# Performance work log

Hardware: AMD Instinct MI355X
Metric: run time of the kernel (lower is better)

Reference implementation:

```python
import jax, jax.numpy as jnp
import numpy as np

N_JETS = 1024
DEPTH = 10
FEATURES = 8
HIDDEN = 128


def setup_inputs() -> dict:
    key = jax.random.key(0)
    keys = jax.random.split(key, DEPTH + 4)
    inp = {}
    for j in range(DEPTH):
        n = N_JETS * (2 ** j)
        inp["contents_%d" % j] = jax.random.normal(keys[j], (n, FEATURES), dtype=jnp.float32)
    for j in range(DEPTH - 1):
        n = N_JETS * (2 ** j)
        # complete binary tree: children of node i at level j are nodes 2i, 2i+1 at level j+1
        inp["children_%d" % j] = jnp.arange(2 * n, dtype=jnp.int32).reshape(n, 2)
    inp["W_u"] = jax.random.normal(keys[DEPTH], (HIDDEN, FEATURES), dtype=jnp.float32) * (1.0 / np.sqrt(FEATURES))
    inp["b_u"] = jnp.zeros((HIDDEN,), dtype=jnp.float32)
    inp["W_h"] = jax.random.normal(keys[DEPTH + 1], (HIDDEN, 3 * HIDDEN), dtype=jnp.float32) * (1.0 / np.sqrt(3 * HIDDEN))
    inp["b_h"] = jnp.zeros((HIDDEN,), dtype=jnp.float32)
    return inp


def _forward(contents, children, W_u, b_u, W_h, b_h):
    # Bottom-up pass: deepest level (leaves) first, exactly as the torch loop
    # over levels[::-1]. All non-leaf nodes are inner (n_inners[j] == n_j).
    emb = None
    L = len(contents)
    for j in reversed(range(L)):
        u = jax.nn.relu(contents[j] @ W_u.T + b_u)  # [n_j, H], fc_u + relu
        if j == L - 1:
            emb = u  # leaf level: no children, embedding is just u_k
        else:
            h_L = emb[children[j][:, 0]]  # gather left child embeddings  [n_j, H]
            h_R = emb[children[j][:, 1]]  # gather right child embeddings [n_j, H]
            h = jnp.concatenate([h_L, h_R, u], axis=1)  # [n_j, 3H]
            emb = jax.nn.relu(h @ W_h.T + b_h)  # fc_h + relu -> [n_j, H]
    return emb.reshape(N_JETS, -1)  # roots, one embedding per jet


def reference(contents_0, contents_1, contents_2, contents_3, contents_4,
              contents_5, contents_6, contents_7, contents_8, contents_9,
              children_0, children_1, children_2, children_3, children_4,
              children_5, children_6, children_7, children_8,
              W_u, b_u, W_h, b_h):
    contents = [contents_0, contents_1, contents_2, contents_3, contents_4,
                contents_5, contents_6, contents_7, contents_8, contents_9]
    children = [children_0, children_1, children_2, children_3, children_4,
                children_5, children_6, children_7, children_8]
    return _forward(contents, children, W_u, b_u, W_h, b_h)
```

## Files before the change

### kernel.cpp

```cpp
#include <hip/hip_runtime.h>
#include <hip/hip_bf16.h>

typedef __attribute__((ext_vector_type(8))) short bf16x8;
typedef __attribute__((ext_vector_type(4))) float f32x4;
typedef __attribute__((ext_vector_type(4))) unsigned short u16x4;

__device__ __forceinline__ unsigned short f2bf(float f) {
    __hip_bfloat16 h = __float2bfloat16(f);
    union { __hip_bfloat16 h; unsigned short u; } v; v.h = h;
    return v.u;
}

__device__ __forceinline__ void cp16_g2l(const void* g, void* l) {
    __builtin_amdgcn_global_load_lds(
        (const __attribute__((address_space(1))) unsigned int*)g,
        (__attribute__((address_space(3))) unsigned int*)l, 16, 0, 0);
}

__global__ __launch_bounds__(384) void k_cvtW(const float* __restrict__ Wh,
                                              unsigned short* __restrict__ Wbf) {
    int n = blockIdx.x, k = threadIdx.x;
    Wbf[n * 384 + k] = f2bf(Wh[n * 384 + k]);
}

__global__ __launch_bounds__(512, 4) void k_main(
    const float* __restrict__ c0, const float* __restrict__ c1,
    const float* __restrict__ c2, const float* __restrict__ c3,
    const float* __restrict__ c4, const float* __restrict__ c5,
    const float* __restrict__ c6, const float* __restrict__ c7,
    const float* __restrict__ c8, const float* __restrict__ c9,
    const unsigned short* __restrict__ Wbf,
    const float* __restrict__ Wu, const float* __restrict__ bu,
    const float* __restrict__ bh,
    unsigned short* __restrict__ tbase,
    float* __restrict__ outF)
{
    __shared__ __align__(16) unsigned short A_lds[2][64][128];
    __shared__ __align__(16) unsigned short u_lds[64][128];
    __shared__ __align__(16) unsigned short wu_lds[8][32][8];

    const int t = threadIdx.x, lane = t & 63, wid = t >> 6;
    const int l15 = lane & 15, l4 = lane >> 4;
    const int wrow = wid & 3;
    const int wcolh = wid >> 2;
    const int b = blockIdx.x;

    bf16x8 wreg[12];
    {
        int n = wid * 16 + l15;
        #pragma unroll
        for (int kb = 0; kb < 12; ++kb)
            wreg[kb] = *reinterpret_cast<const bf16x8*>(Wbf + n * 384 + kb * 32 + l4 * 8);
    }
    #pragma unroll
    for (int kb = 0; kb < 12; ++kb)
        asm volatile("" : "+v"(wreg[kb]));

    if (wid == 0 && l4 < 2) {
        #pragma unroll
        for (int nf = 0; nf < 8; ++nf) {
            int n = nf * 16 + l15;
            bf16x8 v = {0, 0, 0, 0, 0, 0, 0, 0};
            if (l4 == 0) {
                #pragma unroll
                for (int k = 0; k < 8; ++k) ((unsigned short*)&v)[k] = f2bf(Wu[n * 8 + k]);
            } else {
                ((unsigned short*)&v)[0] = f2bf(bu[n]);
            }
            *(bf16x8*)&wu_lds[nf][l4 * 16 + l15][0] = v;
        }
    }
    const f32x4 bh4 = *(const f32x4*)&bh[wid * 16 + l4 * 4];

    bf16x8 zeroA = {0, 0, 0, 0, 0, 0, 0, 0};
    bf16x8 onesA = zeroA; ((unsigned short*)&onesA)[0] = 0x3F80;

    __syncthreads();

    #define RG(j) (tbase + (size_t)131072 * (512 - (2 << (j))))

    f32x4 cO0 = {0,0,0,0}, cO1 = {0,0,0,0};

    {
        const int T = 8;
        const int tb = b * T;
        unsigned short* eOut = RG(8);
        if (l4 == 0) {
            const float* p = c8 + ((size_t)tb * 64 + wrow * 16 + l15) * 8;
            cO0 = *(const f32x4*)p; cO1 = *(const f32x4*)(p + 4);
        }
        for (int tt = 0; tt < T; ++tt) {
            const int tile = tb + tt;
            {
                bf16x8 cb = zeroA;
                if (l4 == 0) {
                    #pragma unroll
                    for (int e = 0; e < 4; ++e) {
                        ((unsigned short*)&cb)[e]     = f2bf(cO0[e]);
                        ((unsigned short*)&cb)[e + 4] = f2bf(cO1[e]);
                    }
                } else if (l4 == 1) cb = onesA;
                const int i = wrow * 16 + l15;
                #pragma unroll
                for (int nfi = 0; nfi < 4; ++nfi) {
                    int nf = wcolh * 4 + nfi;
                    bf16x8 wv = zeroA;
                    if (l4 < 2) wv = *(const bf16x8*)&wu_lds[nf][l4 * 16 + l15][0];
                    f32x4 z = {0.f, 0.f, 0.f, 0.f};
                    z = __builtin_amdgcn_mfma_f32_16x16x32_bf16(wv, cb, z, 0, 0, 0);
                    u16x4 pk;
                    #pragma unroll
                    for (int r = 0; r < 4; ++r) pk[r] = f2bf(fmaxf(z[r], 0.f));
                    int n4 = nf * 16 + l4 * 4;
                    *(u16x4*)&u_lds[i][n4 ^ ((i & 15) << 3)] = pk;
                }
            }
            {
                const float* pcBase = c9 + ((size_t)tile * 128 + wrow * 32 + l15) * 8;
                #pragma unroll
                for (int rb = 0; rb < 2; ++rb) {
                    bf16x8 cb = zeroA;
                    if (l4 == 0) {
                        f32x4 a  = *(const f32x4*)(pcBase + rb * 128);
                        f32x4 b2 = *(const f32x4*)(pcBase + rb * 128 + 4);
                        #pragma unroll
                        for (int e = 0; e < 4; ++e) {
                            ((unsigned short*)&cb)[e]     = f2bf(a[e]);
                            ((unsigned short*)&cb)[e + 4] = f2bf(b2[e]);
                        }
                    } else if (l4 == 1) cb = onesA;
                    const int rr = wrow * 32 + rb * 16 + l15;
                    const int cc = rr & 1, il = rr >> 1;
                    #pragma unroll
                    for (int nfi = 0; nfi < 4; ++nfi) {
                        int nf = wcolh * 4 + nfi;
                        bf16x8 wv = zeroA;
                        if (l4 < 2) wv = *(const bf16x8*)&wu_lds[nf][l4 * 16 + l15][0];
                        f32x4 z = {0.f, 0.f, 0.f, 0.f};
                        z = __builtin_amdgcn_mfma_f32_16x16x32_bf16(wv, cb, z, 0, 0, 0);
                        u16x4 pk;
                        #pragma unroll
                        for (int r = 0; r < 4; ++r) pk[r] = f2bf(fmaxf(z[r], 0.f));
                        int n4 = nf * 16 + l4 * 4;
                        *(u16x4*)&A_lds[cc][il][n4 ^ ((il & 15) << 3)] = pk;
                    }
                }
            }
            {
                int tn = (tt + 1 < T) ? tile + 1 : tile;
                if (l4 == 0) {
                    const float* p = c8 + ((size_t)tn * 64 + wrow * 16 + l15) * 8;
                    cO0 = *(const f32x4*)p; cO1 = *(const f32x4*)(p + 4);
                }
            }
            asm volatile("s_waitcnt lgkmcnt(0)" ::: "memory");
            __builtin_amdgcn_sched_barrier(0);
            __builtin_amdgcn_s_barrier();
            __builtin_amdgcn_sched_barrier(0);

            f32x4 acc[4];
            #pragma unroll
            for (int mf = 0; mf < 4; ++mf) acc[mf] = bh4;
            #pragma unroll
            for (int kb = 0; kb < 8; ++kb) {
                bf16x8 af[4];
                #pragma unroll
                for (int mf = 0; mf < 4; ++mf) {
                    int i = mf * 16 + l15;
                    af[mf] = *(const bf16x8*)&A_lds[kb >> 2][i][((((kb & 3) * 4) + l4) ^ (i & 15)) * 8];
                }
                #pragma unroll
                for (int mf = 0; mf < 4; ++mf)
                    acc[mf] = __builtin_amdgcn_mfma_f32_16x16x32_bf16(wreg[kb], af[mf], acc[mf], 0, 0, 0);
            }
            #pragma unroll
            for (int kb = 8; kb < 12; ++kb) {
                bf16x8 af[4];
                #pragma unroll
                for (int mf = 0; mf < 4; ++mf) {
                    int i = mf * 16 + l15;
                    af[mf] = *(const bf16x8*)&u_lds[i][((((kb - 8) * 4) + l4) ^ (i & 15)) * 8];
                }
                #pragma unroll
                for (int mf = 0; mf < 4; ++mf)
                    acc[mf] = __builtin_amdgcn_mfma_f32_16x16x32_bf16(wreg[kb], af[mf], acc[mf], 0, 0, 0);
            }
            #pragma unroll
            for (int mf = 0; mf < 4; ++mf) {
                int i = mf * 16 + l15;
                int Rg = tile * 64 + i;
                int rr = Rg & 127, cc = rr & 1, il = rr >> 1;
                u16x4 pk;
                #pragma unroll
                for (int r = 0; r < 4; ++r) pk[r] = f2bf(fmaxf(acc[mf][r], 0.f));
                int n4 = wid * 16 + l4 * 4;
                *(u16x4*)&eOut[(size_t)(Rg >> 7) * 16384 + cc * 8192 + il * 128
                               + (n4 ^ ((il & 15) << 3))] = pk;
            }
            asm volatile("s_waitcnt lgkmcnt(0)" ::: "memory");
            __builtin_amdgcn_sched_barrier(0);
            __builtin_amdgcn_s_barrier();
        }
        asm volatile("s_waitcnt vmcnt(0) lgkmcnt(0)" ::: "memory");
        __builtin_amdgcn_sched_barrier(0);
        __builtin_amdgcn_s_barrier();
    }

    for (int j = 7; j >= 5; --j) {
        const int T = 1 << (j - 5);
        const int tb = b * T;
        const float* contO = (j == 7) ? c7 : (j == 6) ? c6 : c5;
        const unsigned short* eIn = RG(j + 1);
        unsigned short* eOut = RG(j);

        {
            const unsigned short* src = eIn + (size_t)tb * 16384;
            #pragma unroll
            for (int it = 0; it < 4; ++it) {
                int q = t + it * 512;
                cp16_g2l(src + q * 8, &A_lds[0][0][0] + q * 8);
            }
            if (l4 == 0) {
                const float* p = contO + ((size_t)tb * 64 + wrow * 16 + l15) * 8;
                cO0 = *(const f32x4*)p; cO1 = *(const f32x4*)(p + 4);
            }
        }
        __syncthreads();

        for (int tt = 0; tt < T; ++tt) {
            const int tile = tb + tt;
            {
                bf16x8 cb = zeroA;
                if (l4 == 0) {
                    #pragma unroll
                    for (int e = 0; e < 4; ++e) {
                        ((unsigned short*)&cb)[e]     = f2bf(cO0[e]);
                        ((unsigned short*)&cb)[e + 4] = f2bf(cO1[e]);
                    }
                } else if (l4 == 1) cb = onesA;
                const int i = wrow * 16 + l15;
                #pragma unroll
                for (int nfi = 0; nfi < 4; ++nfi) {
                    int nf = wcolh * 4 + nfi;
                    bf16x8 wv = zeroA;
                    if (l4 < 2) wv = *(const bf16x8*)&wu_lds[nf][l4 * 16 + l15][0];
                    f32x4 z = {0.f, 0.f, 0.f, 0.f};
                    z = __builtin_amdgcn_mfma_f32_16x16x32_bf16(wv, cb, z, 0, 0, 0);
                    u16x4 pk;
                    #pragma unroll
                    for (int r = 0; r < 4; ++r) pk[r] = f2bf(fmaxf(z[r], 0.f));
                    int n4 = nf * 16 + l4 * 4;
                    *(u16x4*)&u_lds[i][n4 ^ ((i & 15) << 3)] = pk;
                }
            }
            {
                int tn = (tt + 1 < T) ? tile + 1 : tile;
                if (l4 == 0) {
                    const float* p = contO + ((size_t)tn * 64 + wrow * 16 + l15) * 8;
                    cO0 = *(const f32x4*)p; cO1 = *(const f32x4*)(p + 4);
                }
            }
            asm volatile("s_waitcnt vmcnt(6)" ::: "memory");
            asm volatile("s_waitcnt lgkmcnt(0)" ::: "memory");
            __builtin_amdgcn_sched_barrier(0);
            __builtin_amdgcn_s_barrier();
            __builtin_amdgcn_sched_barrier(0);

            f32x4 acc[4];
            #pragma unroll
            for (int mf = 0; mf < 4; ++mf) acc[mf] = bh4;
            #pragma unroll
            for (int kb = 0; kb < 8; ++kb) {
                bf16x8 af[4];
                #pragma unroll
                for (int mf = 0; mf < 4; ++mf) {
                    int i = mf * 16 + l15;
                    af[mf] = *(const bf16x8*)&A_lds[kb >> 2][i][((((kb & 3) * 4) + l4) ^ (i & 15)) * 8];
                }
                #pragma unroll
                for (int mf = 0; mf < 4; ++mf)
                    acc[mf] = __builtin_amdgcn_mfma_f32_16x16x32_bf16(wreg[kb], af[mf], acc[mf], 0, 0, 0);
            }
            asm volatile("s_waitcnt lgkmcnt(0)" ::: "memory");
            __builtin_amdgcn_sched_barrier(0);
            __builtin_amdgcn_s_barrier();
            __builtin_amdgcn_sched_barrier(0);
            if (tt + 1 < T) {
                const unsigned short* src = eIn + (size_t)(tile + 1) * 16384;
                #pragma unroll
                for (int it = 0; it < 4; ++it) {
                    int q = t + it * 512;
                    cp16_g2l(src + q * 8, &A_lds[0][0][0] + q * 8);
                }
            }
            #pragma unroll
            for (int kb = 8; kb < 12; ++kb) {
                bf16x8 af[4];
                #pragma unroll
                for (int mf = 0; mf < 4; ++mf) {
                    int i = mf * 16 + l15;
                    af[mf] = *(const bf16x8*)&u_lds[i][((((kb - 8) * 4) + l4) ^ (i & 15)) * 8];
                }
                #pragma unroll
                for (int mf = 0; mf < 4; ++mf)
                    acc[mf] = __builtin_amdgcn_mfma_f32_16x16x32_bf16(wreg[kb], af[mf], acc[mf], 0, 0, 0);
            }
            #pragma unroll
            for (int mf = 0; mf < 4; ++mf) {
                int i = mf * 16 + l15;
                int Rg = tile * 64 + i;
                int rr = Rg & 127, cc = rr & 1, il = rr >> 1;
                u16x4 pk;
                #pragma unroll
                for (int r = 0; r < 4; ++r) pk[r] = f2bf(fmaxf(acc[mf][r], 0.f));
                int n4 = wid * 16 + l4 * 4;
                *(u16x4*)&eOut[(size_t)(Rg >> 7) * 16384 + cc * 8192 + il * 128
                               + (n4 ^ ((il & 15) << 3))] = pk;
            }
            asm volatile("s_waitcnt lgkmcnt(0)" ::: "memory");
            __builtin_amdgcn_sched_barrier(0);
            __builtin_amdgcn_s_barrier();
        }
        asm volatile("s_waitcnt vmcnt(0) lgkmcnt(0)" ::: "memory");
        __builtin_amdgcn_sched_barrier(0);
        __builtin_amdgcn_s_barrier();
    }

    for (int j = 4; j >= 0; --j) {
        const int R = 2 << j;
        const float* contO = (j == 4) ? c4 : (j == 3) ? c3 : (j == 2) ? c2
                           : (j == 1) ? c1 : c0;
        const unsigned short* eIn = RG(j + 1);
        unsigned short* eOut = (j > 0) ? RG(j) : nullptr;

        const size_t rowBase  = (size_t)b * (size_t)R;
        const size_t crowBase = rowBase * 2;

        {
            const int ilBase = ((int)(crowBase & 127)) >> 1;
            const unsigned short* gb = eIn + (crowBase >> 7) * (size_t)16384
                                     + (size_t)ilBase * 128;
            const int per = R * 16;
            for (int q = t; q < 2 * per; q += 512) {
                int cc = (q >= per) ? 1 : 0;
                int qq = q - cc * per;
                int il = qq >> 4, slot = qq & 15;
                int kc  = slot ^ (il & 15);
                int src = kc ^ ((ilBase + il) & 15);
                bf16x8 v = *(const bf16x8*)(gb + (size_t)cc * 8192 + il * 128 + src * 8);
                *(bf16x8*)&A_lds[cc][il][slot * 8] = v;
            }
        }
        {
            f32x4 a0 = {0,0,0,0}, a1 = {0,0,0,0};
            if (l4 == 0) {
                size_t row = rowBase + (size_t)(wrow * 16 + l15);
                size_t mx = rowBase + R - 1; if (row > mx) row = mx;
                const float* p = contO + row * 8;
                a0 = *(const f32x4*)p; a1 = *(const f32x4*)(p + 4);
            }
            bf16x8 cb = zeroA;
            if (l4 == 0) {
                #pragma unroll
                for (int e = 0; e < 4; ++e) {
                    ((unsigned short*)&cb)[e]     = f2bf(a0[e]);
                    ((unsigned short*)&cb)[e + 4] = f2bf(a1[e]);
                }
            } else if (l4 == 1) cb = onesA;
            const int i = wrow * 16 + l15;
            #pragma unroll
            for (int nfi = 0; nfi < 4; ++nfi) {
                int nf = wcolh * 4 + nfi;
                bf16x8 wv = zeroA;
                if (l4 < 2) wv = *(const bf16x8*)&wu_lds[nf][l4 * 16 + l15][0];
                f32x4 z = {0.f, 0.f, 0.f, 0.f};
                z = __builtin_amdgcn_mfma_f32_16x16x32_bf16(wv, cb, z, 0, 0, 0);
                u16x4 pk;
                #pragma unroll
                for (int r = 0; r < 4; ++r) pk[r] = f2bf(fmaxf(z[r], 0.f));
                int n4 = nf * 16 + l4 * 4;
                *(u16x4*)&u_lds[i][n4 ^ ((i & 15) << 3)] = pk;
            }
        }
        asm volatile("s_waitcnt lgkmcnt(0)" ::: "memory");
        __builtin_amdgcn_sched_barrier(0);
        __builtin_amdgcn_s_barrier();
        __builtin_amdgcn_sched_barrier(0);

        f32x4 acc[4];
        #pragma unroll
        for (int mf = 0; mf < 4; ++mf) acc[mf] = bh4;
        #pragma unroll
        for (int kb = 0; kb < 8; ++kb) {
            bf16x8 af[4];
            #pragma unroll
            for (int mf = 0; mf < 4; ++mf) {
                int i = mf * 16 + l15;
                af[mf] = *(const bf16x8*)&A_lds[kb >> 2][i][((((kb & 3) * 4) + l4) ^ (i & 15)) * 8];
            }
            #pragma unroll
            for (int mf = 0; mf < 4; ++mf)
                acc[mf] = __builtin_amdgcn_mfma_f32_16x16x32_bf16(wreg[kb], af[mf], acc[mf], 0, 0, 0);
        }
        #pragma unroll
        for (int kb = 8; kb < 12; ++kb) {
            bf16x8 af[4];
            #pragma unroll
            for (int mf = 0; mf < 4; ++mf) {
                int i = mf * 16 + l15;
                af[mf] = *(const bf16x8*)&u_lds[i][((((kb - 8) * 4) + l4) ^ (i & 15)) * 8];
            }
            #pragma unroll
            for (int mf = 0; mf < 4; ++mf)
                acc[mf] = __builtin_amdgcn_mfma_f32_16x16x32_bf16(wreg[kb], af[mf], acc[mf], 0, 0, 0);
        }
        if (j == 0) {
            #pragma unroll
            for (int mf = 0; mf < 4; ++mf) {
                int i = mf * 16 + l15;
                if (i < R) {
                    f32x4 o;
                    #pragma unroll
                    for (int r = 0; r < 4; ++r) o[r] = fmaxf(acc[mf][r], 0.f);
                    *(f32x4*)&outF[(rowBase + i) * 128 + wid * 16 + l4 * 4] = o;
                }
            }
        } else {
            #pragma unroll
            for (int mf = 0; mf < 4; ++mf) {
                int i = mf * 16 + l15;
                if (i < R) {
                    size_t Rg = rowBase + i;
                    int rr = (int)(Rg & 127), cc = rr & 1, il = rr >> 1;
                    u16x4 pk;
                    #pragma unroll
                    for (int r = 0; r < 4; ++r) pk[r] = f2bf(fmaxf(acc[mf][r], 0.f));
                    int n4 = wid * 16 + l4 * 4;
                    *(u16x4*)&eOut[(Rg >> 7) * 16384 + cc * 8192 + il * 128
                                   + (n4 ^ ((il & 15) << 3))] = pk;
                }
            }
        }
        asm volatile("s_waitcnt vmcnt(0) lgkmcnt(0)" ::: "memory");
        __builtin_amdgcn_sched_barrier(0);
        __builtin_amdgcn_s_barrier();
    }
    #undef RG
}

extern "C" void kernel_launch(void* const* d_in, const int* in_sizes, int n_in,
                              void* d_out, int out_size, void* d_ws, size_t ws_size,
                              hipStream_t stream) {
    const float* c[10];
    for (int j = 0; j < 10; ++j) c[j] = (const float*)d_in[j];
    const float* Wu = (const float*)d_in[19];
    const float* bu = (const float*)d_in[20];
    const float* Wh = (const float*)d_in[21];
    const float* bh = (const float*)d_in[22];

    unsigned short* Wbf   = (unsigned short*)d_ws;
    unsigned short* tbase = (unsigned short*)((char*)d_ws + (1u << 20));

    k_cvtW<<<128, 384, 0, stream>>>(Wh, Wbf);
    k_main<<<512, 512, 0, stream>>>(c[0], c[1], c[2], c[3], c[4], c[5], c[6], c[7],
                                    c[8], c[9], Wbf, Wu, bu, bh, tbase, (float*)d_out);
}
```

Measured before the change: 125.2 us.

## Fuse level 8 into level 7 via LDS, keep W_u in registers

Level-8 embeddings are now computed into a second LDS buffer and consumed directly by the level-7 GEMM in the same block, so the level-8 global round trip and its phase disappear. W_u and bias fragments are held in registers instead of being read from LDS on every small MFMA, and repeated code is factored into lambdas. The cost is a larger LDS footprint, which may lower occupancy, plus extra barriers per sub-tile.

```diff
diff --git a/kernel.cpp b/kernel.cpp
--- a/kernel.cpp
+++ b/kernel.cpp
@@ -35,14 +35,13 @@
     unsigned short* __restrict__ tbase,
     float* __restrict__ outF)
 {
-    __shared__ __align__(16) unsigned short A_lds[2][64][128];
+    __shared__ __align__(16) unsigned short A_c9[2][64][128];
+    __shared__ __align__(16) unsigned short A8[2][64][128];
     __shared__ __align__(16) unsigned short u_lds[64][128];
-    __shared__ __align__(16) unsigned short wu_lds[8][32][8];
 
     const int t = threadIdx.x, lane = t & 63, wid = t >> 6;
     const int l15 = lane & 15, l4 = lane >> 4;
-    const int wrow = wid & 3;
-    const int wcolh = wid >> 2;
+    const int wrow = wid & 3, wcolh = wid >> 2;
     const int b = blockIdx.x;
 
     bf16x8 wreg[12];
@@ -56,39 +55,189 @@
     for (int kb = 0; kb < 12; ++kb)
         asm volatile("" : "+v"(wreg[kb]));
 
-    if (wid == 0 && l4 < 2) {
-        #pragma unroll
-        for (int nf = 0; nf < 8; ++nf) {
-            int n = nf * 16 + l15;
-            bf16x8 v = {0, 0, 0, 0, 0, 0, 0, 0};
-            if (l4 == 0) {
-                #pragma unroll
-                for (int k = 0; k < 8; ++k) ((unsigned short*)&v)[k] = f2bf(Wu[n * 8 + k]);
-            } else {
-                ((unsigned short*)&v)[0] = f2bf(bu[n]);
-            }
-            *(bf16x8*)&wu_lds[nf][l4 * 16 + l15][0] = v;
-        }
-    }
+    bf16x8 wureg[4];
+    #pragma unroll
+    for (int nfi = 0; nfi < 4; ++nfi) {
+        int n = (wcolh * 4 + nfi) * 16 + l15;
+        bf16x8 v = {0, 0, 0, 0, 0, 0, 0, 0};
+        if (l4 == 0) {
+            #pragma unroll
+            for (int k = 0; k < 8; ++k) ((unsigned short*)&v)[k] = f2bf(Wu[n * 8 + k]);
+        } else if (l4 == 1) {
+            ((unsigned short*)&v)[0] = f2bf(bu[n]);
+        }
+        wureg[nfi] = v;
+    }
+    #pragma unroll
+    for (int nfi = 0; nfi < 4; ++nfi)
+        asm volatile("" : "+v"(wureg[nfi]));
+
     const f32x4 bh4 = *(const f32x4*)&bh[wid * 16 + l4 * 4];
-
     bf16x8 zeroA = {0, 0, 0, 0, 0, 0, 0, 0};
     bf16x8 onesA = zeroA; ((unsigned short*)&onesA)[0] = 0x3F80;
 
-    __syncthreads();
-
     #define RG(j) (tbase + (size_t)131072 * (512 - (2 << (j))))
-
-    f32x4 cO0 = {0,0,0,0}, cO1 = {0,0,0,0};
+    #define BAR_LGKM() do { asm volatile("s_waitcnt lgkmcnt(0)" ::: "memory"); \
+        __builtin_amdgcn_sched_barrier(0); __builtin_amdgcn_s_barrier(); \
+        __builtin_amdgcn_sched_barrier(0); } while (0)
+
+    auto UPH = [&](const float* contO, size_t row0, size_t rowMax) {
+        bf16x8 cb = zeroA;
+        if (l4 == 0) {
+            size_t row = row0 + (size_t)(wrow * 16 + l15);
+            if (row > rowMax) row = rowMax;
+            const float* p = contO + row * 8;
+            f32x4 a0 = *(const f32x4*)p, a1 = *(const f32x4*)(p + 4);
+            #pragma unroll
+            for (int e = 0; e < 4; ++e) {
+                ((unsigned short*)&cb)[e]     = f2bf(a0[e]);
+                ((unsigned short*)&cb)[e + 4] = f2bf(a1[e]);
+            }
+        } else if (l4 == 1) cb = onesA;
+        const int i = wrow * 16 + l15;
+        #pragma unroll
+        for (int nfi = 0; nfi < 4; ++nfi) {
+            f32x4 z = {0.f, 0.f, 0.f, 0.f};
+            z = __builtin_amdgcn_mfma_f32_16x16x32_bf16(wureg[nfi], cb, z, 0, 0, 0);
+            u16x4 pk;
+            #pragma unroll
+            for (int r = 0; r < 4; ++r) pk[r] = f2bf(fmaxf(z[r], 0.f));
+            int n4 = (wcolh * 4 + nfi) * 16 + l4 * 4;
+            *(u16x4*)&u_lds[i][n4 ^ ((i & 15) << 3)] = pk;
+        }
+    };
+    auto GEMM_A = [&](const unsigned short (*A)[64][128], f32x4* acc) {
+        #pragma unroll
+        for (int mf = 0; mf < 4; ++mf) acc[mf] = bh4;
+        #pragma unroll
+        for (int kb = 0; kb < 8; ++kb) {
+            bf16x8 af[4];
+            #pragma unroll
+            for (int mf = 0; mf < 4; ++mf) {
+                int i = mf * 16 + l15;
+                af[mf] = *(const bf16x8*)&A[kb >> 2][i][((((kb & 3) * 4) + l4) ^ (i & 15)) * 8];
+            }
+            #pragma unroll
+            for (int mf = 0; mf < 4; ++mf)
+                acc[mf] = __builtin_amdgcn_mfma_f32_16x16x32_bf16(wreg[kb], af[mf], acc[mf], 0, 0, 0);
+        }
+    };
+    auto GEMM_U = [&](f32x4* acc) {
+        #pragma unroll
+        for (int kb = 8; kb < 12; ++kb) {
+            bf16x8 af[4];
+            #pragma unroll
+            for (int mf = 0; mf < 4; ++mf) {
+                int i = mf * 16 + l15;
+                af[mf] = *(const bf16x8*)&u_lds[i][((((kb - 8) * 4) + l4) ^ (i & 15)) * 8];
+            }
+            #pragma unroll
+            for (int mf = 0; mf < 4; ++mf)
+                acc[mf] = __builtin_amdgcn_mfma_f32_16x16x32_bf16(wreg[kb], af[mf], acc[mf], 0, 0, 0);
+        }
+    };
 
     {
-        const int T = 8;
+        unsigned short* e7 = RG(7);
+        for (int q = 0; q < 4; ++q) {
+            const int tile7 = b * 4 + q;
+            for (int s = 0; s < 2; ++s) {
+                const size_t tile8 = (size_t)tile7 * 2 + s;
+                UPH(c8, tile8 * 64, tile8 * 64 + 63);
+                {
+                    const float* pcBase = c9 + (tile8 * 128 + (size_t)(wrow * 32 + l15)) * 8;
+                    #pragma unroll
+                    for (int rb = 0; rb < 2; ++rb) {
+                        bf16x8 cb = zeroA;
+                        if (l4 == 0) {
+                            f32x4 a  = *(const f32x4*)(pcBase + rb * 128);
+                            f32x4 b2 = *(const f32x4*)(pcBase + rb * 128 + 4);
+                            #pragma unroll
+                            for (int e = 0; e < 4; ++e) {
+                                ((unsigned short*)&cb)[e]     = f2bf(a[e]);
+                                ((unsigned short*)&cb)[e + 4] = f2bf(b2[e]);
+                            }
+                        } else if (l4 == 1) cb = onesA;
+                        const int rr = wrow * 32 + rb * 16 + l15;
+                        const int cc = rr & 1, il = rr >> 1;
+                        #pragma unroll
+                        for (int nfi = 0; nfi < 4; ++nfi) {
+                            f32x4 z = {0.f, 0.f, 0.f, 0.f};
+                            z = __builtin_amdgcn_mfma_f32_16x16x32_bf16(wureg[nfi], cb, z, 0, 0, 0);
+                            u16x4 pk;
+                            #pragma unroll
+                            for (int r = 0; r < 4; ++r) pk[r] = f2bf(fmaxf(z[r], 0.f));
+                            int n4 = (wcolh * 4 + nfi) * 16 + l4 * 4;
+                            *(u16x4*)&A_c9[cc][il][n4 ^ ((il & 15) << 3)] = pk;
+                        }
+                    }
+                }
+                BAR_LGKM();
+                {
+                    f32x4 acc[4];
+                    GEMM_A(A_c9, acc);
+                    GEMM_U(acc);
+                    #pragma unroll
+                    for (int mf = 0; mf < 4; ++mf) {
+                        int i = mf * 16 + l15;
+                        int cc = i & 1, il = s * 32 + (i >> 1);
+                        u16x4 pk;
+                        #pragma unroll
+                        for (int r = 0; r < 4; ++r) pk[r] = f2bf(fmaxf(acc[mf][r], 0.f));
+                        int n4 = wid * 16 + l4 * 4;
+                        *(u16x4*)&A8[cc][il][n4 ^ ((il & 15) << 3)] = pk;
+                    }
+                }
+                BAR_LGKM();
+            }
+            UPH(c7, (size_t)tile7 * 64, (size_t)tile7 * 64 + 63);
+            BAR_LGKM();
+            {
+                f32x4 acc[4];
+                GEMM_A(A8, acc);
+                GEMM_U(acc);
+                #pragma unroll
+                for (int mf = 0; mf < 4; ++mf) {
+                    int i = mf * 16 + l15;
+                    int Rg = tile7 * 64 + i;
+                    int rr = Rg & 127, cc = rr & 1, il = rr >> 1;
+                    u16x4 pk;
+                    #pragma unroll
+                    for (int r = 0; r < 4; ++r) pk[r] = f2bf(fmaxf(acc[mf][r], 0.f));
+                    int n4 = wid * 16 + l4 * 4;
+                    *(u16x4*)&e7[(size_t)(Rg >> 7) * 16384 + cc * 8192 + il * 128
+                                 + (n4 ^ ((il & 15) << 3))] = pk;
+                }
+            }
+            BAR_LGKM();
+        }
+        asm volatile("s_waitcnt vmcnt(0) lgkmcnt(0)" ::: "memory");
+        __builtin_amdgcn_sched_barrier(0);
+        __builtin_amdgcn_s_barrier();
+    }
+
+    for (int j = 6; j >= 5; --j) {
+        const int T = 1 << (j - 5);
         const int tb = b * T;
-        unsigned short* eOut = RG(8);
-        if (l4 == 0) {
-            const float* p = c8 + ((size_t)tb * 64 + wrow * 16 + l15) * 8;
-            cO0 = *(const f32x4*)p; cO1 = *(const f32x4*)(p + 4);
-        }
+        const float* contO = (j == 6) ? c6 : c5;
+        const unsigned short* eIn = RG(j + 1);
+        unsigned short* eOut = RG(j);
+
+        f32x4 cO0 = {0,0,0,0}, cO1 = {0,0,0,0};
+        {
+            const unsigned short* src = eIn + (size_t)tb * 16384;
+            #pragma unroll
+            for (int it = 0; it < 4; ++it) {
+                int q = t + it * 512;
+                cp16_g2l(src + q * 8, &A_c9[0][0][0] + q * 8);
+            }
+            if (l4 == 0) {
+                const float* p = contO + ((size_t)tb * 64 + wrow * 16 + l15) * 8;
+                cO0 = *(const f32x4*)p; cO1 = *(const f32x4*)(p + 4);
+            }
+        }
+        __syncthreads();
+
         for (int tt = 0; tt < T; ++tt) {
             const int tile = tb + tt;
             {
@@ -103,153 +252,12 @@
                 const int i = wrow * 16 + l15;
                 #pragma unroll
                 for (int nfi = 0; nfi < 4; ++nfi) {
-                    int nf = wcolh * 4 + nfi;
-                    bf16x8 wv = zeroA;
-                    if (l4 < 2) wv = *(const bf16x8*)&wu_lds[nf][l4 * 16 + l15][0];
                     f32x4 z = {0.f, 0.f, 0.f, 0.f};
-                    z = __builtin_amdgcn_mfma_f32_16x16x32_bf16(wv, cb, z, 0, 0, 0);
+                    z = __builtin_amdgcn_mfma_f32_16x16x32_bf16(wureg[nfi], cb, z, 0, 0, 0);
                     u16x4 pk;
                     #pragma unroll
                     for (int r = 0; r < 4; ++r) pk[r] = f2bf(fmaxf(z[r], 0.f));
-                    int n4 = nf * 16 + l4 * 4;
-                    *(u16x4*)&u_lds[i][n4 ^ ((i & 15) << 3)] = pk;
-                }
-            }
-            {
-                const float* pcBase = c9 + ((size_t)tile * 128 + wrow * 32 + l15) * 8;
-                #pragma unroll
-                for (int rb = 0; rb < 2; ++rb) {
-                    bf16x8 cb = zeroA;
-                    if (l4 == 0) {
-                        f32x4 a  = *(const f32x4*)(pcBase + rb * 128);
-                        f32x4 b2 = *(const f32x4*)(pcBase + rb * 128 + 4);
-                        #pragma unroll
-                        for (int e = 0; e < 4; ++e) {
-                            ((unsigned short*)&cb)[e]     = f2bf(a[e]);
-                            ((unsigned short*)&cb)[e + 4] = f2bf(b2[e]);
-                        }
-                    } else if (l4 == 1) cb = onesA;
-                    const int rr = wrow * 32 + rb * 16 + l15;
-                    const int cc = rr & 1, il = rr >> 1;
-                    #pragma unroll
-                    for (int nfi = 0; nfi < 4; ++nfi) {
-                        int nf = wcolh * 4 + nfi;
-                        bf16x8 wv = zeroA;
-                        if (l4 < 2) wv = *(const bf16x8*)&wu_lds[nf][l4 * 16 + l15][0];
-                        f32x4 z = {0.f, 0.f, 0.f, 0.f};
-                        z = __builtin_amdgcn_mfma_f32_16x16x32_bf16(wv, cb, z, 0, 0, 0);
-                        u16x4 pk;
-                        #pragma unroll
-                        for (int r = 0; r < 4; ++r) pk[r] = f2bf(fmaxf(z[r], 0.f));
-                        int n4 = nf * 16 + l4 * 4;
-                        *(u16x4*)&A_lds[cc][il][n4 ^ ((il & 15) << 3)] = pk;
-                    }
-                }
-            }
-            {
-                int tn = (tt + 1 < T) ? tile + 1 : tile;
-                if (l4 == 0) {
-                    const float* p = c8 + ((size_t)tn * 64 + wrow * 16 + l15) * 8;
-                    cO0 = *(const f32x4*)p; cO1 = *(const f32x4*)(p + 4);
-                }
-            }
-            asm volatile("s_waitcnt lgkmcnt(0)" ::: "memory");
-            __builtin_amdgcn_sched_barrier(0);
-            __builtin_amdgcn_s_barrier();
-            __builtin_amdgcn_sched_barrier(0);
-
-            f32x4 acc[4];
-            #pragma unroll
-            for (int mf = 0; mf < 4; ++mf) acc[mf] = bh4;
-            #pragma unroll
-            for (int kb = 0; kb < 8; ++kb) {
-                bf16x8 af[4];
-                #pragma unroll
-                for (int mf = 0; mf < 4; ++mf) {
-                    int i = mf * 16 + l15;
-                    af[mf] = *(const bf16x8*)&A_lds[kb >> 2][i][((((kb & 3) * 4) + l4) ^ (i & 15)) * 8];
-                }
-                #pragma unroll
-                for (int mf = 0; mf < 4; ++mf)
-                    acc[mf] = __builtin_amdgcn_mfma_f32_16x16x32_bf16(wreg[kb], af[mf], acc[mf], 0, 0, 0);
-            }
-            #pragma unroll
-            for (int kb = 8; kb < 12; ++kb) {
-                bf16x8 af[4];
-                #pragma unroll
-                for (int mf = 0; mf < 4; ++mf) {
-                    int i = mf * 16 + l15;
-                    af[mf] = *(const bf16x8*)&u_lds[i][((((kb - 8) * 4) + l4) ^ (i & 15)) * 8];
-                }
-                #pragma unroll
-                for (int mf = 0; mf < 4; ++mf)
-                    acc[mf] = __builtin_amdgcn_mfma_f32_16x16x32_bf16(wreg[kb], af[mf], acc[mf], 0, 0, 0);
-            }
-            #pragma unroll
-            for (int mf = 0; mf < 4; ++mf) {
-                int i = mf * 16 + l15;
-                int Rg = tile * 64 + i;
-                int rr = Rg & 127, cc = rr & 1, il = rr >> 1;
-                u16x4 pk;
-                #pragma unroll
-                for (int r = 0; r < 4; ++r) pk[r] = f2bf(fmaxf(acc[mf][r], 0.f));
-                int n4 = wid * 16 + l4 * 4;
-                *(u16x4*)&eOut[(size_t)(Rg >> 7) * 16384 + cc * 8192 + il * 128
-                               + (n4 ^ ((il & 15) << 3))] = pk;
-            }
-            asm volatile("s_waitcnt lgkmcnt(0)" ::: "memory");
-            __builtin_amdgcn_sched_barrier(0);
-            __builtin_amdgcn_s_barrier();
-        }
-        asm volatile("s_waitcnt vmcnt(0) lgkmcnt(0)" ::: "memory");
-        __builtin_amdgcn_sched_barrier(0);
-        __builtin_amdgcn_s_barrier();
-    }
-
-    for (int j = 7; j >= 5; --j) {
-        const int T = 1 << (j - 5);
-        const int tb = b * T;
-        const float* contO = (j == 7) ? c7 : (j == 6) ? c6 : c5;
-        const unsigned short* eIn = RG(j + 1);
-        unsigned short* eOut = RG(j);
-
-        {
-            const unsigned short* src = eIn + (size_t)tb * 16384;
-            #pragma unroll
-            for (int it = 0; it < 4; ++it) {
-                int q = t + it * 512;
-                cp16_g2l(src + q * 8, &A_lds[0][0][0] + q * 8);
-            }
-            if (l4 == 0) {
-                const float* p = contO + ((size_t)tb * 64 + wrow * 16 + l15) * 8;
-                cO0 = *(const f32x4*)p; cO1 = *(const f32x4*)(p + 4);
-            }
-        }
-        __syncthreads();
-
-        for (int tt = 0; tt < T; ++tt) {
-            const int tile = tb + tt;
-            {
-                bf16x8 cb = zeroA;
-                if (l4 == 0) {
-                    #pragma unroll
-                    for (int e = 0; e < 4; ++e) {
-                        ((unsigned short*)&cb)[e]     = f2bf(cO0[e]);
-                        ((unsigned short*)&cb)[e + 4] = f2bf(cO1[e]);
-                    }
-                } else if (l4 == 1) cb = onesA;
-                const int i = wrow * 16 + l15;
-                #pragma unroll
-                for (int nfi = 0; nfi < 4; ++nfi) {
-                    int nf = wcolh * 4 + nfi;
-                    bf16x8 wv = zeroA;
-                    if (l4 < 2) wv = *(const bf16x8*)&wu_lds[nf][l4 * 16 + l15][0];
-                    f32x4 z = {0.f, 0.f, 0.f, 0.f};
-                    z = __builtin_amdgcn_mfma_f32_16x16x32_bf16(wv, cb, z, 0, 0, 0);
-                    u16x4 pk;
-                    #pragma unroll
-                    for (int r = 0; r < 4; ++r) pk[r] = f2bf(fmaxf(z[r], 0.f));
-                    int n4 = nf * 16 + l4 * 4;
+                    int n4 = (wcolh * 4 + nfi) * 16 + l4 * 4;
                     *(u16x4*)&u_lds[i][n4 ^ ((i & 15) << 3)] = pk;
                 }
             }
@@ -261,50 +269,20 @@
                 }
             }
             asm volatile("s_waitcnt vmcnt(6)" ::: "memory");
-            asm volatile("s_waitcnt lgkmcnt(0)" ::: "memory");
-            __builtin_amdgcn_sched_barrier(0);
-            __builtin_amdgcn_s_barrier();
-            __builtin_amdgcn_sched_barrier(0);
+            BAR_LGKM();
 
             f32x4 acc[4];
-            #pragma unroll
-            for (int mf = 0; mf < 4; ++mf) acc[mf] = bh4;
-            #pragma unroll
-            for (int kb = 0; kb < 8; ++kb) {
-                bf16x8 af[4];
-                #pragma unroll
-                for (int mf = 0; mf < 4; ++mf) {
-                    int i = mf * 16 + l15;
-                    af[mf] = *(const bf16x8*)&A_lds[kb >> 2][i][((((kb & 3) * 4) + l4) ^ (i & 15)) * 8];
-                }
-                #pragma unroll
-                for (int mf = 0; mf < 4; ++mf)
-                    acc[mf] = __builtin_amdgcn_mfma_f32_16x16x32_bf16(wreg[kb], af[mf], acc[mf], 0, 0, 0);
-            }
-            asm volatile("s_waitcnt lgkmcnt(0)" ::: "memory");
-            __builtin_amdgcn_sched_barrier(0);
-            __builtin_amdgcn_s_barrier();
-            __builtin_amdgcn_sched_barrier(0);
+            GEMM_A(A_c9, acc);
+            BAR_LGKM();
             if (tt + 1 < T) {
                 const unsigned short* src = eIn + (size_t)(tile + 1) * 16384;
                 #pragma unroll
                 for (int it = 0; it < 4; ++it) {
                     int q = t + it * 512;
-                    cp16_g2l(src + q * 8, &A_lds[0][0][0] + q * 8);
-                }
-            }
-            #pragma unroll
-            for (int kb = 8; kb < 12; ++kb) {
-                bf16x8 af[4];
-                #pragma unroll
-                for (int mf = 0; mf < 4; ++mf) {
-                    int i = mf * 16 + l15;
-                    af[mf] = *(const bf16x8*)&u_lds[i][((((kb - 8) * 4) + l4) ^ (i & 15)) * 8];
-                }
-                #pragma unroll
-                for (int mf = 0; mf < 4; ++mf)
-                    acc[mf] = __builtin_amdgcn_mfma_f32_16x16x32_bf16(wreg[kb], af[mf], acc[mf], 0, 0, 0);
-            }
+                    cp16_g2l(src + q * 8, &A_c9[0][0][0] + q * 8);
+                }
+            }
+            GEMM_U(acc);
             #pragma unroll
             for (int mf = 0; mf < 4; ++mf) {
                 int i = mf * 16 + l15;
@@ -348,72 +326,16 @@
                 int kc  = slot ^ (il & 15);
                 int src = kc ^ ((ilBase + il) & 15);
                 bf16x8 v = *(const bf16x8*)(gb + (size_t)cc * 8192 + il * 128 + src * 8);
-                *(bf16x8*)&A_lds[cc][il][slot * 8] = v;
-            }
-        }
-        {
-            f32x4 a0 = {0,0,0,0}, a1 = {0,0,0,0};
-            if (l4 == 0) {
-                size_t row = rowBase + (size_t)(wrow * 16 + l15);
-                size_t mx = rowBase + R - 1; if (row > mx) row = mx;
-                const float* p = contO + row * 8;
-                a0 = *(const f32x4*)p; a1 = *(const f32x4*)(p + 4);
-            }
-            bf16x8 cb = zeroA;
-            if (l4 == 0) {
-                #pragma unroll
-                for (int e = 0; e < 4; ++e) {
-                    ((unsigned short*)&cb)[e]     = f2bf(a0[e]);
-                    ((unsigned short*)&cb)[e + 4] = f2bf(a1[e]);
-                }
-            } else if (l4 == 1) cb = onesA;
-            const int i = wrow * 16 + l15;
-            #pragma unroll
-            for (int nfi = 0; nfi < 4; ++nfi) {
-                int nf = wcolh * 4 + nfi;
-                bf16x8 wv = zeroA;
-                if (l4 < 2) wv = *(const bf16x8*)&wu_lds[nf][l4 * 16 + l15][0];
-                f32x4 z = {0.f, 0.f, 0.f, 0.f};
-                z = __builtin_amdgcn_mfma_f32_16x16x32_bf16(wv, cb, z, 0, 0, 0);
-                u16x4 pk;
-                #pragma unroll
-                for (int r = 0; r < 4; ++r) pk[r] = f2bf(fmaxf(z[r], 0.f));
-                int n4 = nf * 16 + l4 * 4;
-                *(u16x4*)&u_lds[i][n4 ^ ((i & 15) << 3)] = pk;
-            }
-        }
-        asm volatile("s_waitcnt lgkmcnt(0)" ::: "memory");
-        __builtin_amdgcn_sched_barrier(0);
-        __builtin_amdgcn_s_barrier();
-        __builtin_amdgcn_sched_barrier(0);
+                *(bf16x8*)&A_c9[cc][il][slot * 8] = v;
+            }
+        }
+        UPH(contO, rowBase, rowBase + R - 1);
+        BAR_LGKM();
 
         f32x4 acc[4];
-        #pragma unroll
-        for (int mf = 0; mf < 4; ++mf) acc[mf] = bh4;
-        #pragma unroll
-        for (int kb = 0; kb < 8; ++kb) {
-            bf16x8 af[4];
-            #pragma unroll
-            for (int mf = 0; mf < 4; ++mf) {
-                int i = mf * 16 + l15;
-                af[mf] = *(const bf16x8*)&A_lds[kb >> 2][i][((((kb & 3) * 4) + l4) ^ (i & 15)) * 8];
-            }
-            #pragma unroll
-            for (int mf = 0; mf < 4; ++mf)
-                acc[mf] = __builtin_amdgcn_mfma_f32_16x16x32_bf16(wreg[kb], af[mf], acc[mf], 0, 0, 0);
-        }
-        #pragma unroll
-        for (int kb = 8; kb < 12; ++kb) {
-            bf16x8 af[4];
-            #pragma unroll
-            for (int mf = 0; mf < 4; ++mf) {
-                int i = mf * 16 + l15;
-                af[mf] = *(const bf16x8*)&u_lds[i][((((kb - 8) * 4) + l4) ^ (i & 15)) * 8];
-            }
-            #pragma unroll
-            for (int mf = 0; mf < 4; ++mf)
-                acc[mf] = __builtin_amdgcn_mfma_f32_16x16x32_bf16(wreg[kb], af[mf], acc[mf], 0, 0, 0);
-        }
+        GEMM_A(A_c9, acc);
+        GEMM_U(acc);
+
         if (j == 0) {
             #pragma unroll
             for (int mf = 0; mf < 4; ++mf) {
@@ -446,6 +368,7 @@
         __builtin_amdgcn_s_barrier();
     }
     #undef RG
+    #undef BAR_LGKM
 }
 
 extern "C" void kernel_launch(void* const* d_in, const int* in_sizes, int n_in,
```

Result: slower. 141.3 us (+12.9%).
